# Kernel tuning notes

Measured on AMD Instinct MI355X. Metric: run time of the kernel, lower is better.

## Reference

```python
import jax, jax.numpy as jnp
import numpy as np

VOXEL_SIZE = 0.2
MAX_SP = 512


def _labels_single(coords):
    # coords: [N, 3] float32
    # torch .long() truncates toward zero; astype(int32) matches for these magnitudes
    vc = (coords / VOXEL_SIZE).astype(jnp.int32)
    ids = vc[:, 0] * 10000 + vc[:, 1] * 100 + vc[:, 2]  # hashed voxel id, [N]
    N = ids.shape[0]

    # torch.unique(return_inverse=True): sorted uniques + inverse indices
    sorted_ids = jnp.sort(ids)
    is_new = jnp.concatenate(
        [jnp.ones((1,), dtype=bool), sorted_ids[1:] != sorted_ids[:-1]]
    )
    rank = jnp.cumsum(is_new.astype(jnp.int32)) - 1  # unique idx per sorted slot
    pos = jnp.searchsorted(sorted_ids, ids, side='left')  # first occurrence
    inverse = rank[pos]  # [N] inverse indices into sorted uniques
    n_unique = rank[-1] + 1

    # torch.bincount(inverse): counts per unique voxel (padded to length N)
    counts = jnp.zeros((N,), jnp.int32).at[inverse].add(1)

    # argsort descending, take top MAX_SP largest voxels; padded slots have
    # n_unique > MAX_SP (the only case this branch is used)
    large = jnp.argsort(-counts)[:MAX_SP]

    # remap loop: labels default 0; points in large[j] get label j.
    remap = jnp.zeros((N,), jnp.int32).at[large].set(
        jnp.arange(MAX_SP, dtype=jnp.int32)
    )
    capped = remap[inverse]

    return jnp.where(n_unique > MAX_SP, capped, inverse)


def setup_inputs() -> dict:
    key = jax.random.key(0)
    coords = jax.random.normal(key, (32, 262144, 3), dtype=jnp.float32) * 2.0
    return {"coordinates": coords}


def reference(coordinates):
    # [B, N] int32 superpoint labels
    return jax.vmap(_labels_single)(coordinates)
```

## Files before the change

### kernel.cpp

```cpp
#include <hip/hip_runtime.h>
#include <stdint.h>


#define BATCHES 32
#define NPTS    (1 << 18)
#define MAX_SP  512
#define NBUK    76
#define BUK_VOX 16384
#define DRANGE  (NBUK * BUK_VOX)
#define OFFSET  (DRANGE / 2)
#define BUK_DW  (BUK_VOX / 4)
#define TIERCAP 18432
#define BPB     64
#define PPB     (NPTS / BPB)

typedef float    f32x4 __attribute__((ext_vector_type(4)));
typedef int      i32x4 __attribute__((ext_vector_type(4)));
typedef uint32_t u32x4 __attribute__((ext_vector_type(4)));

__device__ __forceinline__ int pidx(float x, float y, float z) {
    int vx = (int)(x / 0.2f);
    int vy = (int)(y / 0.2f);
    int vz = (int)(z / 0.2f);
    int id = vx * 10000 + vy * 100 + vz;
    int idx = id + OFFSET;
    idx = idx < 0 ? 0 : (idx >= DRANGE ? DRANGE - 1 : idx);
    return idx;
}

__global__ void __launch_bounds__(1024) vidx_count(
    const float* __restrict__ coords, int* __restrict__ vidx,
    int* __restrict__ blkcnt)
{
    int b = blockIdx.x >> 6, blk = blockIdx.x & 63, tid = threadIdx.x;
    __shared__ int cnt[NBUK];
    if (tid < NBUK) cnt[tid] = 0;
    __syncthreads();
    size_t p0 = (size_t)b * NPTS + (size_t)blk * PPB + (size_t)tid * 4;
    const f32x4* cp = (const f32x4*)(coords + p0 * 3);
    f32x4 a = __builtin_nontemporal_load(cp + 0);
    f32x4 c = __builtin_nontemporal_load(cp + 1);
    f32x4 d = __builtin_nontemporal_load(cp + 2);
    i32x4 iv;
    iv[0] = pidx(a[0], a[1], a[2]);
    iv[1] = pidx(a[3], c[0], c[1]);
    iv[2] = pidx(c[2], c[3], d[0]);
    iv[3] = pidx(d[1], d[2], d[3]);
    __builtin_nontemporal_store(iv, (i32x4*)(vidx + p0));
    atomicAdd(&cnt[iv[0] >> 14], 1);
    atomicAdd(&cnt[iv[1] >> 14], 1);
    atomicAdd(&cnt[iv[2] >> 14], 1);
    atomicAdd(&cnt[iv[3] >> 14], 1);
    __syncthreads();
    if (tid < NBUK) blkcnt[blockIdx.x * NBUK + tid] = cnt[tid];
}

__global__ void __launch_bounds__(128) scan64(
    const int* __restrict__ blkcnt, int* __restrict__ blkbase,
    int* __restrict__ bukbase, int* __restrict__ buktot)
{
    int b = blockIdx.x, tid = threadIdx.x;
    __shared__ int c[BPB * NBUK];
    __shared__ int start[NBUK];
    for (int i = tid; i < BPB * NBUK; i += 128)
        c[i] = blkcnt[(size_t)b * BPB * NBUK + i];
    __syncthreads();
    if (tid < NBUK) {
        int s = 0;
        for (int blk = 0; blk < BPB; ++blk) s += c[blk * NBUK + tid];
        buktot[b * NBUK + tid] = s;
        start[tid] = s;
    }
    __syncthreads();
    if (tid == 0) {
        int run = 0;
        for (int k = 0; k < NBUK; ++k) { int t = start[k]; start[k] = run; run += t; }
    }
    __syncthreads();
    if (tid < NBUK) {
        int run = start[tid];
        bukbase[b * NBUK + tid] = run;
        for (int blk = 0; blk < BPB; ++blk) {
            blkbase[((size_t)b * BPB + blk) * NBUK + tid] = run;
            run += c[blk * NBUK + tid];
        }
    }
}

__global__ void __launch_bounds__(1024) scatter4(
    const int* __restrict__ vidx, const int* __restrict__ blkcnt,
    const int* __restrict__ blkbase, int* __restrict__ lists)
{
    int b = blockIdx.x >> 6, tid = threadIdx.x;
    __shared__ int stage[PPB];
    __shared__ int offs[NBUK];
    __shared__ int cur[NBUK];
    __shared__ int rebase[NBUK];
    if (tid < NBUK) offs[tid] = blkcnt[blockIdx.x * NBUK + tid];
    __syncthreads();
    if (tid == 0) {
        int run = 0;
        for (int k = 0; k < NBUK; ++k) { int t = offs[k]; offs[k] = run; run += t; }
    }
    __syncthreads();
    if (tid < NBUK) {
        cur[tid] = offs[tid];
        rebase[tid] = blkbase[blockIdx.x * NBUK + tid] - offs[tid];
    }
    __syncthreads();
    size_t p0 = (size_t)b * NPTS + (size_t)(blockIdx.x & 63) * PPB + (size_t)tid * 4;
    i32x4 iv = __builtin_nontemporal_load((const i32x4*)(vidx + p0));
    #pragma unroll
    for (int j = 0; j < 4; ++j) {
        int idx = iv[j];
        stage[atomicAdd(&cur[idx >> 14], 1)] = idx;
    }
    __syncthreads();
    int* lb = lists + (size_t)b * NPTS;
    #pragma unroll
    for (int j = 0; j < 4; ++j) {
        int i = j * 1024 + tid;
        int v = stage[i];
        __builtin_nontemporal_store(v, &lb[rebase[v >> 14] + i]);
    }
}

__global__ void __launch_bounds__(1024) bucket_hist(
    const int* __restrict__ lists, const int* __restrict__ bukbase,
    const int* __restrict__ buktot, int* __restrict__ bhist)
{
    int k = blockIdx.x, b = blockIdx.y, tid = threadIdx.x;
    __shared__ uint32_t cnt[BUK_DW];
    __shared__ uint32_t h8[8 * 256];
    for (int i = tid; i < BUK_DW; i += 1024) cnt[i] = 0;
    for (int i = tid; i < 8 * 256; i += 1024) h8[i] = 0;
    __syncthreads();
    int st = bukbase[b * NBUK + k], n = buktot[b * NBUK + k];
    const int* seg = lists + (size_t)b * NPTS + st;
    for (int i = tid; i < n; i += 1024) {
        int idx = seg[i] & (BUK_VOX - 1);
        atomicAdd(&cnt[idx >> 2], 1u << ((idx & 3) * 8));
    }
    __syncthreads();
    int rep = (tid >> 7) & 7;
    for (int i = tid; i < BUK_DW; i += 1024) {
        uint32_t w = cnt[i];
        if (w) {
            #pragma unroll
            for (int j = 0; j < 4; ++j) {
                uint32_t cc = (w >> (j * 8)) & 255u;
                if (cc) atomicAdd(&h8[rep * 256 + cc], 1u);
            }
        }
    }
    __syncthreads();
    if (tid < 256) {
        uint32_t s = 0;
        #pragma unroll
        for (int r = 0; r < 8; ++r) s += h8[r * 256 + tid];
        bhist[((size_t)b * NBUK + k) * 256 + tid] = (int)s;
    }
}

__global__ void __launch_bounds__(256) select_params(
    const int* __restrict__ bhist, int* __restrict__ params,
    int* __restrict__ wbase, int* __restrict__ tbase)
{
    int b = blockIdx.x, tid = threadIdx.x;
    __shared__ int tot[256];
    __shared__ int wc_[NBUK], tc_[NBUK];
    __shared__ int sh_T;
    int s = 0;
    for (int k = 0; k < NBUK; ++k) s += bhist[((size_t)b * NBUK + k) * 256 + tid];
    tot[tid] = s;
    __syncthreads();
    if (tid == 0) {
        int nu = 0;
        for (int c = 1; c < 256; ++c) nu += tot[c];
        int acc = 0, c = 255;
        while (c > 1 && acc + tot[c] < MAX_SP) { acc += tot[c]; --c; }
        int T = c, A = acc;
        int m = MAX_SP - A; if (m > tot[T]) m = tot[T];
        params[b * 8 + 0] = T;  params[b * 8 + 1] = A;
        params[b * 8 + 2] = m;  params[b * 8 + 3] = nu;
        params[b * 8 + 4] = A + m;
        sh_T = T;
    }
    __syncthreads();
    int T = sh_T;
    if (tid < NBUK) {
        int ws = 0;
        const int* bh = bhist + ((size_t)b * NBUK + tid) * 256;
        for (int c = T + 1; c < 256; ++c) ws += bh[c];
        wc_[tid] = ws;
        tc_[tid] = bh[T];
    }
    __syncthreads();
    if (tid == 0) {
        int aw = 0, at = 0;
        for (int k = 0; k < NBUK; ++k) {
            wbase[b * NBUK + k] = aw; tbase[b * NBUK + k] = at;
            aw += wc_[k]; at += tc_[k];
        }
    }
}

__global__ void __launch_bounds__(512) collect2(
    const int* __restrict__ lists, const int* __restrict__ bukbase,
    const int* __restrict__ buktot, const int* __restrict__ params,
    const int* __restrict__ wbase, const int* __restrict__ tbase,
    uint32_t* __restrict__ wid, int* __restrict__ wcnt, uint32_t* __restrict__ tier)
{
    int k = blockIdx.x, b = blockIdx.y, tid = threadIdx.x;
    int T = params[b * 8 + 0], m = params[b * 8 + 2];
    int wb = wbase[b * NBUK + k], tb = tbase[b * NBUK + k];
    __shared__ uint32_t cnt[BUK_DW];
    __shared__ int tl[512];
    __shared__ int wpos;
    for (int i = tid; i < BUK_DW; i += 512) cnt[i] = 0;
    if (tid == 0) wpos = 0;
    __syncthreads();
    int st = bukbase[b * NBUK + k], n = buktot[b * NBUK + k];
    const int* seg = lists + (size_t)b * NPTS + st;
    for (int i = tid; i < n; i += 512) {
        int idx = seg[i] & (BUK_VOX - 1);
        atomicAdd(&cnt[idx >> 2], 1u << ((idx & 3) * 8));
    }
    __syncthreads();
    u32x4 v[2];
    v[0] = ((const u32x4*)cnt)[tid * 2 + 0];
    v[1] = ((const u32x4*)cnt)[tid * 2 + 1];
    int base_id = (k * BUK_DW + tid * 8) * 4;
    int ntier = 0;
    #pragma unroll
    for (int q = 0; q < 2; ++q) {
        #pragma unroll
        for (int d = 0; d < 4; ++d) {
            uint32_t w = v[q][d];
            if (!w) continue;
            #pragma unroll
            for (int j = 0; j < 4; ++j) {
                int c = (int)((w >> (j * 8)) & 255u);
                if (c > T) {
                    int p = atomicAdd(&wpos, 1);
                    wid [b * MAX_SP + wb + p] = (uint32_t)(base_id + (q * 4 + d) * 4 + j);
                    wcnt[b * MAX_SP + wb + p] = c;
                } else if (c == T) ++ntier;
            }
        }
    }
    tl[tid] = ntier;
    __syncthreads();
    if (tb < m && ntier > 0) {
        int pre = 0;
        for (int j = 0; j < 512; ++j) { int t = tl[j]; if (j < tid) pre += t; }
        int pos = tb + pre, kk = 0;
        #pragma unroll
        for (int q = 0; q < 2; ++q) {
            #pragma unroll
            for (int d = 0; d < 4; ++d) {
                uint32_t w = v[q][d];
                if (!w) continue;
                #pragma unroll
                for (int j = 0; j < 4; ++j) {
                    int c = (int)((w >> (j * 8)) & 255u);
                    if (c == T) {
                        int q2 = pos + kk; ++kk;
                        if (q2 < TIERCAP) tier[b * TIERCAP + q2] = (uint32_t)(base_id + (q * 4 + d) * 4 + j);
                    }
                }
            }
        }
    }
}

__global__ void __launch_bounds__(512) rank512(
    const int* __restrict__ params, const uint32_t* __restrict__ wid,
    const int* __restrict__ wcnt, const uint32_t* __restrict__ tier,
    uint32_t* __restrict__ lookup)
{
    int b = blockIdx.x, tid = threadIdx.x;
    int T = params[b * 8 + 0], A = params[b * 8 + 1];
    int nu = params[b * 8 + 3], nw = params[b * 8 + 4];
    __shared__ uint32_t wu[MAX_SP];
    __shared__ int      wc[MAX_SP];
    if (tid < A)       { wu[tid] = wid[b * MAX_SP + tid]; wc[tid] = wcnt[b * MAX_SP + tid]; }
    else if (tid < nw) { wu[tid] = tier[b * TIERCAP + (tid - A)]; wc[tid] = T; }
    __syncthreads();
    if (tid < nw) {
        uint32_t u = wu[tid]; int c = wc[tid];
        int r = 0, ur = 0;
        for (int j = 0; j < nw; ++j) {
            uint32_t uj = wu[j]; int cj = wc[j];
            r  += ((cj > c) || (cj == c && uj < u)) ? 1 : 0;
            ur += (uj < u) ? 1 : 0;
        }
        int label = (nu <= MAX_SP) ? ur : r;
        lookup[b * MAX_SP + ur] = (u << 9) | (uint32_t)label;
    }
}

__global__ void __launch_bounds__(1024) write_labels4(
    const int* __restrict__ vidx, const int* __restrict__ params,
    const uint32_t* __restrict__ lookup, int* __restrict__ out)
{
    __shared__ uint32_t lu[MAX_SP];
    int b = blockIdx.x >> 6, tid = threadIdx.x;
    if (tid < MAX_SP) lu[tid] = lookup[b * MAX_SP + tid];
    __syncthreads();
    int nw = params[b * 8 + 4];
    size_t p0 = (size_t)b * NPTS + (size_t)(blockIdx.x & 63) * PPB + (size_t)tid * 4;
    i32x4 iv = __builtin_nontemporal_load((const i32x4*)(vidx + p0));
    i32x4 ov;
    #pragma unroll
    for (int j = 0; j < 4; ++j) {
        uint32_t u = (uint32_t)iv[j];
        int lo = 0, hi = nw;
        while (lo < hi) { int mid = (lo + hi) >> 1; if ((lu[mid] >> 9) < u) lo = mid + 1; else hi = mid; }
        int label = 0;
        if (lo < nw && (lu[lo] >> 9) == u) label = (int)(lu[lo] & 511u);
        ov[j] = label;
    }
    __builtin_nontemporal_store(ov, (i32x4*)(out + p0));
}

extern "C" void kernel_launch(void* const* d_in, const int* in_sizes, int n_in,
                              void* d_out, int out_size, void* d_ws, size_t ws_size,
                              hipStream_t stream) {
    const float* coords = (const float*)d_in[0];
    int* out = (int*)d_out;

    uint8_t* p = (uint8_t*)d_ws;
    int*      vidx    = (int*)p;      p += (size_t)BATCHES * NPTS * 4;
    int*      lists   = (int*)p;      p += (size_t)BATCHES * NPTS * 4;
    int*      blkcnt  = (int*)p;      p += (size_t)BATCHES * BPB * NBUK * 4;
    int*      blkbase = (int*)p;      p += (size_t)BATCHES * BPB * NBUK * 4;
    int*      bhist   = (int*)p;      p += (size_t)BATCHES * NBUK * 256 * 4;
    uint32_t* tier    = (uint32_t*)p; p += (size_t)BATCHES * TIERCAP * 4;
    int*      bukbase = (int*)p;      p += (size_t)BATCHES * NBUK * 4;
    int*      buktot  = (int*)p;      p += (size_t)BATCHES * NBUK * 4;
    int*      wbase   = (int*)p;      p += (size_t)BATCHES * NBUK * 4;
    int*      tbase   = (int*)p;      p += (size_t)BATCHES * NBUK * 4;
    int*      params  = (int*)p;      p += (size_t)BATCHES * 8 * 4;
    uint32_t* wid     = (uint32_t*)p; p += (size_t)BATCHES * MAX_SP * 4;
    int*      wcnt    = (int*)p;      p += (size_t)BATCHES * MAX_SP * 4;
    uint32_t* lookup  = (uint32_t*)p; p += (size_t)BATCHES * MAX_SP * 4;

    vidx_count   <<<BATCHES * BPB, 1024, 0, stream>>>(coords, vidx, blkcnt);
    scan64       <<<BATCHES, 128, 0, stream>>>(blkcnt, blkbase, bukbase, buktot);
    scatter4     <<<BATCHES * BPB, 1024, 0, stream>>>(vidx, blkcnt, blkbase, lists);
    bucket_hist  <<<dim3(NBUK, BATCHES), 1024, 0, stream>>>(lists, bukbase, buktot, bhist);
    select_params<<<BATCHES, 256, 0, stream>>>(bhist, params, wbase, tbase);
    collect2     <<<dim3(NBUK, BATCHES), 512, 0, stream>>>(lists, bukbase, buktot, params, wbase, tbase, wid, wcnt, tier);
    rank512      <<<BATCHES, 512, 0, stream>>>(params, wid, wcnt, tier, lookup);
    write_labels4<<<BATCHES * BPB, 1024, 0, stream>>>(vidx, params, lookup, out);
}
```

Measured before the change: 327.2 us.

## Emit compacted voxel-count pairs in bucket_hist and reuse them in collect2

bucket_hist now packs each nonzero voxel of its bucket into an (id<<8 | count) word. It places these in a per-batch pairs buffer using a wave shuffle scan plus a global atomic cursor, and records the base and length for each bucket. collect2 reads these pairs instead of re-reading the bucket's point list and rebuilding the per-voxel LDS histogram with atomics. This is meant to remove the redundant second histogram pass. The cost is an extra scattered write of the pairs, a per-batch cursor reset in scan64, and chunked per-thread reads in collect2 that are not coalesced.

New measurement: 335.6 us. 2.5% more time.

```diff
diff --git a/kernel.cpp b/kernel.cpp
--- a/kernel.cpp
+++ b/kernel.cpp
@@ -57,11 +57,13 @@
 
 __global__ void __launch_bounds__(128) scan64(
     const int* __restrict__ blkcnt, int* __restrict__ blkbase,
-    int* __restrict__ bukbase, int* __restrict__ buktot)
+    int* __restrict__ bukbase, int* __restrict__ buktot,
+    int* __restrict__ paircur)
 {
     int b = blockIdx.x, tid = threadIdx.x;
     __shared__ int c[BPB * NBUK];
     __shared__ int start[NBUK];
+    if (tid == 0) paircur[b] = 0;
     for (int i = tid; i < BPB * NBUK; i += 128)
         c[i] = blkcnt[(size_t)b * BPB * NBUK + i];
     __syncthreads();
@@ -127,11 +129,15 @@
 
 __global__ void __launch_bounds__(1024) bucket_hist(
     const int* __restrict__ lists, const int* __restrict__ bukbase,
-    const int* __restrict__ buktot, int* __restrict__ bhist)
+    const int* __restrict__ buktot, int* __restrict__ bhist,
+    uint32_t* __restrict__ pairs, int* __restrict__ paircur,
+    int* __restrict__ pairbase, int* __restrict__ pairn)
 {
     int k = blockIdx.x, b = blockIdx.y, tid = threadIdx.x;
     __shared__ uint32_t cnt[BUK_DW];
     __shared__ uint32_t h8[8 * 256];
+    __shared__ int woff[16];
+    __shared__ int sbase;
     for (int i = tid; i < BUK_DW; i += 1024) cnt[i] = 0;
     for (int i = tid; i < 8 * 256; i += 1024) h8[i] = 0;
     __syncthreads();
@@ -142,15 +148,48 @@
         atomicAdd(&cnt[idx >> 2], 1u << ((idx & 3) * 8));
     }
     __syncthreads();
+    u32x4 w4 = ((const u32x4*)cnt)[tid];
     int rep = (tid >> 7) & 7;
-    for (int i = tid; i < BUK_DW; i += 1024) {
-        uint32_t w = cnt[i];
-        if (w) {
-            #pragma unroll
-            for (int j = 0; j < 4; ++j) {
-                uint32_t cc = (w >> (j * 8)) & 255u;
-                if (cc) atomicAdd(&h8[rep * 256 + cc], 1u);
-            }
+    int nz = 0;
+    #pragma unroll
+    for (int d = 0; d < 4; ++d) {
+        uint32_t w = w4[d];
+        if (!w) continue;
+        #pragma unroll
+        for (int j = 0; j < 4; ++j) {
+            uint32_t cc = (w >> (j * 8)) & 255u;
+            if (cc) { ++nz; atomicAdd(&h8[rep * 256 + cc], 1u); }
+        }
+    }
+    int lane = tid & 63, wv = tid >> 6;
+    int inc = nz;
+    #pragma unroll
+    for (int s = 1; s < 64; s <<= 1) {
+        int y = __shfl_up(inc, s);
+        if (lane >= s) inc += y;
+    }
+    int pre = inc - nz;
+    if (lane == 63) woff[wv] = inc;
+    __syncthreads();
+    if (tid == 0) {
+        int run = 0;
+        for (int i = 0; i < 16; ++i) { int t = woff[i]; woff[i] = run; run += t; }
+        sbase = atomicAdd(&paircur[b], run);
+        pairbase[b * NBUK + k] = sbase;
+        pairn[b * NBUK + k] = run;
+    }
+    __syncthreads();
+    int off = sbase + woff[wv] + pre;
+    uint32_t* pp = pairs + (size_t)b * NPTS;
+    int base_id = k * BUK_VOX + tid * 16;
+    #pragma unroll
+    for (int d = 0; d < 4; ++d) {
+        uint32_t w = w4[d];
+        if (!w) continue;
+        #pragma unroll
+        for (int j = 0; j < 4; ++j) {
+            uint32_t cc = (w >> (j * 8)) & 255u;
+            if (cc) pp[off++] = ((uint32_t)(base_id + d * 4 + j) << 8) | cc;
         }
     }
     __syncthreads();
@@ -206,48 +245,31 @@
 }
 
 __global__ void __launch_bounds__(512) collect2(
-    const int* __restrict__ lists, const int* __restrict__ bukbase,
-    const int* __restrict__ buktot, const int* __restrict__ params,
+    const uint32_t* __restrict__ pairs, const int* __restrict__ pairbase,
+    const int* __restrict__ pairn, const int* __restrict__ params,
     const int* __restrict__ wbase, const int* __restrict__ tbase,
     uint32_t* __restrict__ wid, int* __restrict__ wcnt, uint32_t* __restrict__ tier)
 {
     int k = blockIdx.x, b = blockIdx.y, tid = threadIdx.x;
     int T = params[b * 8 + 0], m = params[b * 8 + 2];
     int wb = wbase[b * NBUK + k], tb = tbase[b * NBUK + k];
-    __shared__ uint32_t cnt[BUK_DW];
+    int pb = pairbase[b * NBUK + k], P = pairn[b * NBUK + k];
+    const uint32_t* pp = pairs + (size_t)b * NPTS + pb;
     __shared__ int tl[512];
     __shared__ int wpos;
-    for (int i = tid; i < BUK_DW; i += 512) cnt[i] = 0;
     if (tid == 0) wpos = 0;
     __syncthreads();
-    int st = bukbase[b * NBUK + k], n = buktot[b * NBUK + k];
-    const int* seg = lists + (size_t)b * NPTS + st;
-    for (int i = tid; i < n; i += 512) {
-        int idx = seg[i] & (BUK_VOX - 1);
-        atomicAdd(&cnt[idx >> 2], 1u << ((idx & 3) * 8));
-    }
-    __syncthreads();
-    u32x4 v[2];
-    v[0] = ((const u32x4*)cnt)[tid * 2 + 0];
-    v[1] = ((const u32x4*)cnt)[tid * 2 + 1];
-    int base_id = (k * BUK_DW + tid * 8) * 4;
+    int C = (P + 511) >> 9;
+    int s0 = tid * C, s1 = s0 + C; if (s1 > P) s1 = P;
     int ntier = 0;
-    #pragma unroll
-    for (int q = 0; q < 2; ++q) {
-        #pragma unroll
-        for (int d = 0; d < 4; ++d) {
-            uint32_t w = v[q][d];
-            if (!w) continue;
-            #pragma unroll
-            for (int j = 0; j < 4; ++j) {
-                int c = (int)((w >> (j * 8)) & 255u);
-                if (c > T) {
-                    int p = atomicAdd(&wpos, 1);
-                    wid [b * MAX_SP + wb + p] = (uint32_t)(base_id + (q * 4 + d) * 4 + j);
-                    wcnt[b * MAX_SP + wb + p] = c;
-                } else if (c == T) ++ntier;
-            }
-        }
+    for (int i = s0; i < s1; ++i) {
+        uint32_t pr = pp[i];
+        int c = (int)(pr & 255u);
+        if (c > T) {
+            int p = atomicAdd(&wpos, 1);
+            wid [b * MAX_SP + wb + p] = pr >> 8;
+            wcnt[b * MAX_SP + wb + p] = c;
+        } else if (c == T) ++ntier;
     }
     tl[tid] = ntier;
     __syncthreads();
@@ -255,20 +277,11 @@
         int pre = 0;
         for (int j = 0; j < 512; ++j) { int t = tl[j]; if (j < tid) pre += t; }
         int pos = tb + pre, kk = 0;
-        #pragma unroll
-        for (int q = 0; q < 2; ++q) {
-            #pragma unroll
-            for (int d = 0; d < 4; ++d) {
-                uint32_t w = v[q][d];
-                if (!w) continue;
-                #pragma unroll
-                for (int j = 0; j < 4; ++j) {
-                    int c = (int)((w >> (j * 8)) & 255u);
-                    if (c == T) {
-                        int q2 = pos + kk; ++kk;
-                        if (q2 < TIERCAP) tier[b * TIERCAP + q2] = (uint32_t)(base_id + (q * 4 + d) * 4 + j);
-                    }
-                }
+        for (int i = s0; i < s1; ++i) {
+            uint32_t pr = pp[i];
+            if ((int)(pr & 255u) == T) {
+                int q2 = pos + kk; ++kk;
+                if (q2 < TIERCAP) tier[b * TIERCAP + q2] = pr >> 8;
             }
         }
     }
@@ -333,6 +346,7 @@
     uint8_t* p = (uint8_t*)d_ws;
     int*      vidx    = (int*)p;      p += (size_t)BATCHES * NPTS * 4;
     int*      lists   = (int*)p;      p += (size_t)BATCHES * NPTS * 4;
+    uint32_t* pairs   = (uint32_t*)p; p += (size_t)BATCHES * NPTS * 4;
     int*      blkcnt  = (int*)p;      p += (size_t)BATCHES * BPB * NBUK * 4;
     int*      blkbase = (int*)p;      p += (size_t)BATCHES * BPB * NBUK * 4;
     int*      bhist   = (int*)p;      p += (size_t)BATCHES * NBUK * 256 * 4;
@@ -341,17 +355,20 @@
     int*      buktot  = (int*)p;      p += (size_t)BATCHES * NBUK * 4;
     int*      wbase   = (int*)p;      p += (size_t)BATCHES * NBUK * 4;
     int*      tbase   = (int*)p;      p += (size_t)BATCHES * NBUK * 4;
+    int*      pairbase= (int*)p;      p += (size_t)BATCHES * NBUK * 4;
+    int*      pairn   = (int*)p;      p += (size_t)BATCHES * NBUK * 4;
+    int*      paircur = (int*)p;      p += (size_t)BATCHES * 4;
     int*      params  = (int*)p;      p += (size_t)BATCHES * 8 * 4;
     uint32_t* wid     = (uint32_t*)p; p += (size_t)BATCHES * MAX_SP * 4;
     int*      wcnt    = (int*)p;      p += (size_t)BATCHES * MAX_SP * 4;
     uint32_t* lookup  = (uint32_t*)p; p += (size_t)BATCHES * MAX_SP * 4;
 
     vidx_count   <<<BATCHES * BPB, 1024, 0, stream>>>(coords, vidx, blkcnt);
-    scan64       <<<BATCHES, 128, 0, stream>>>(blkcnt, blkbase, bukbase, buktot);
+    scan64       <<<BATCHES, 128, 0, stream>>>(blkcnt, blkbase, bukbase, buktot, paircur);
     scatter4     <<<BATCHES * BPB, 1024, 0, stream>>>(vidx, blkcnt, blkbase, lists);
-    bucket_hist  <<<dim3(NBUK, BATCHES), 1024, 0, stream>>>(lists, bukbase, buktot, bhist);
+    bucket_hist  <<<dim3(NBUK, BATCHES), 1024, 0, stream>>>(lists, bukbase, buktot, bhist, pairs, paircur, pairbase, pairn);
     select_params<<<BATCHES, 256, 0, stream>>>(bhist, params, wbase, tbase);
-    collect2     <<<dim3(NBUK, BATCHES), 512, 0, stream>>>(lists, bukbase, buktot, params, wbase, tbase, wid, wcnt, tier);
+    collect2     <<<dim3(NBUK, BATCHES), 512, 0, stream>>>(pairs, pairbase, pairn, params, wbase, tbase, wid, wcnt, tier);
     rank512      <<<BATCHES, 512, 0, stream>>>(params, wid, wcnt, tier, lookup);
     write_labels4<<<BATCHES * BPB, 1024, 0, stream>>>(vidx, params, lookup, out);
 }
```

## Persist per-bucket packed voxel counts and reuse them in collect instead of recounting

Applied to the files above, without the earlier changes.

bucket_hist now writes its packed 8-bit per-voxel shared-memory counts to a global scratch buffer. collect2 reads those counts directly instead of re-reading the bucket lists and rebuilding the histogram with shared atomics. The serial 512-element prefix loop in collect2 is also replaced by a wavefront shuffle scan plus per-wave offsets. This adds a 16 KB-per-bucket global write and read (about 160 MB total) in exchange for removing a second full pass over the lists and its atomics.

After: 315.0 us. 3.7% less time.

```diff
diff --git a/kernel.cpp b/kernel.cpp
--- a/kernel.cpp
+++ b/kernel.cpp
@@ -127,7 +127,8 @@
 
 __global__ void __launch_bounds__(1024) bucket_hist(
     const int* __restrict__ lists, const int* __restrict__ bukbase,
-    const int* __restrict__ buktot, int* __restrict__ bhist)
+    const int* __restrict__ buktot, int* __restrict__ bhist,
+    uint32_t* __restrict__ cnt16k)
 {
     int k = blockIdx.x, b = blockIdx.y, tid = threadIdx.x;
     __shared__ uint32_t cnt[BUK_DW];
@@ -142,15 +143,17 @@
         atomicAdd(&cnt[idx >> 2], 1u << ((idx & 3) * 8));
     }
     __syncthreads();
+    u32x4 w4 = ((const u32x4*)cnt)[tid];
+    ((u32x4*)(cnt16k + (size_t)(b * NBUK + k) * BUK_DW))[tid] = w4;
     int rep = (tid >> 7) & 7;
-    for (int i = tid; i < BUK_DW; i += 1024) {
-        uint32_t w = cnt[i];
-        if (w) {
-            #pragma unroll
-            for (int j = 0; j < 4; ++j) {
-                uint32_t cc = (w >> (j * 8)) & 255u;
-                if (cc) atomicAdd(&h8[rep * 256 + cc], 1u);
-            }
+    #pragma unroll
+    for (int d = 0; d < 4; ++d) {
+        uint32_t w = w4[d];
+        if (!w) continue;
+        #pragma unroll
+        for (int j = 0; j < 4; ++j) {
+            uint32_t cc = (w >> (j * 8)) & 255u;
+            if (cc) atomicAdd(&h8[rep * 256 + cc], 1u);
         }
     }
     __syncthreads();
@@ -206,30 +209,21 @@
 }
 
 __global__ void __launch_bounds__(512) collect2(
-    const int* __restrict__ lists, const int* __restrict__ bukbase,
-    const int* __restrict__ buktot, const int* __restrict__ params,
+    const uint32_t* __restrict__ cnt16k, const int* __restrict__ params,
     const int* __restrict__ wbase, const int* __restrict__ tbase,
     uint32_t* __restrict__ wid, int* __restrict__ wcnt, uint32_t* __restrict__ tier)
 {
     int k = blockIdx.x, b = blockIdx.y, tid = threadIdx.x;
     int T = params[b * 8 + 0], m = params[b * 8 + 2];
     int wb = wbase[b * NBUK + k], tb = tbase[b * NBUK + k];
-    __shared__ uint32_t cnt[BUK_DW];
-    __shared__ int tl[512];
+    __shared__ int woff[8];
     __shared__ int wpos;
-    for (int i = tid; i < BUK_DW; i += 512) cnt[i] = 0;
     if (tid == 0) wpos = 0;
-    __syncthreads();
-    int st = bukbase[b * NBUK + k], n = buktot[b * NBUK + k];
-    const int* seg = lists + (size_t)b * NPTS + st;
-    for (int i = tid; i < n; i += 512) {
-        int idx = seg[i] & (BUK_VOX - 1);
-        atomicAdd(&cnt[idx >> 2], 1u << ((idx & 3) * 8));
-    }
-    __syncthreads();
+    const u32x4* g = (const u32x4*)(cnt16k + (size_t)(b * NBUK + k) * BUK_DW);
     u32x4 v[2];
-    v[0] = ((const u32x4*)cnt)[tid * 2 + 0];
-    v[1] = ((const u32x4*)cnt)[tid * 2 + 1];
+    v[0] = g[tid * 2 + 0];
+    v[1] = g[tid * 2 + 1];
+    __syncthreads();
     int base_id = (k * BUK_DW + tid * 8) * 4;
     int ntier = 0;
     #pragma unroll
@@ -249,11 +243,18 @@
             }
         }
     }
-    tl[tid] = ntier;
-    __syncthreads();
+    int lane = tid & 63, wv = tid >> 6;
+    int inc = ntier;
+    #pragma unroll
+    for (int s = 1; s < 64; s <<= 1) {
+        int y = __shfl_up(inc, s);
+        if (lane >= s) inc += y;
+    }
+    if (lane == 63) woff[wv] = inc;
+    __syncthreads();
+    int pre = inc - ntier;
+    for (int i = 0; i < wv; ++i) pre += woff[i];
     if (tb < m && ntier > 0) {
-        int pre = 0;
-        for (int j = 0; j < 512; ++j) { int t = tl[j]; if (j < tid) pre += t; }
         int pos = tb + pre, kk = 0;
         #pragma unroll
         for (int q = 0; q < 2; ++q) {
@@ -333,6 +334,7 @@
     uint8_t* p = (uint8_t*)d_ws;
     int*      vidx    = (int*)p;      p += (size_t)BATCHES * NPTS * 4;
     int*      lists   = (int*)p;      p += (size_t)BATCHES * NPTS * 4;
+    uint32_t* cnt16k  = (uint32_t*)p; p += (size_t)BATCHES * NBUK * BUK_DW * 4;
     int*      blkcnt  = (int*)p;      p += (size_t)BATCHES * BPB * NBUK * 4;
     int*      blkbase = (int*)p;      p += (size_t)BATCHES * BPB * NBUK * 4;
     int*      bhist   = (int*)p;      p += (size_t)BATCHES * NBUK * 256 * 4;
@@ -349,9 +351,9 @@
     vidx_count   <<<BATCHES * BPB, 1024, 0, stream>>>(coords, vidx, blkcnt);
     scan64       <<<BATCHES, 128, 0, stream>>>(blkcnt, blkbase, bukbase, buktot);
     scatter4     <<<BATCHES * BPB, 1024, 0, stream>>>(vidx, blkcnt, blkbase, lists);
-    bucket_hist  <<<dim3(NBUK, BATCHES), 1024, 0, stream>>>(lists, bukbase, buktot, bhist);
+    bucket_hist  <<<dim3(NBUK, BATCHES), 1024, 0, stream>>>(lists, bukbase, buktot, bhist, cnt16k);
     select_params<<<BATCHES, 256, 0, stream>>>(bhist, params, wbase, tbase);
-    collect2     <<<dim3(NBUK, BATCHES), 512, 0, stream>>>(lists, bukbase, buktot, params, wbase, tbase, wid, wcnt, tier);
+    collect2     <<<dim3(NBUK, BATCHES), 512, 0, stream>>>(cnt16k, params, wbase, tbase, wid, wcnt, tier);
     rank512      <<<BATCHES, 512, 0, stream>>>(params, wid, wcnt, tier, lookup);
     write_labels4<<<BATCHES * BPB, 1024, 0, stream>>>(vidx, params, lookup, out);
 }
```
